# Optimization experiments

Measured on AMD Instinct MI355X. Metric: run time of the kernel, lower is better.

The kernel has to match this reference:

```python
import jax, jax.numpy as jnp
import numpy as np

B, IN, H, NC = 8192, 1024, 1024, 16
CS = H // NC  # chunk_size = 64


def cumsoftmax(x):
    # cumulative softmax along last dim
    return jnp.cumsum(jax.nn.softmax(x, axis=-1), axis=-1)


def setup_inputs() -> dict:
    key = jax.random.key(0)
    ks = jax.random.split(key, 9)
    s_ih = 1.0 / np.sqrt(IN)
    s_hh = 1.0 / np.sqrt(H)
    return {
        "x": jax.random.normal(ks[0], (B, IN), jnp.float32),
        "hx": jax.random.normal(ks[1], (B, H), jnp.float32),
        "cx": jax.random.normal(ks[2], (B, NC, CS), jnp.float32),
        "input_floor": jax.random.normal(ks[3], (B, NC), jnp.float32),
        "forget_floor": jax.random.normal(ks[4], (B, NC), jnp.float32),
        "W_ih": jax.random.uniform(ks[5], (4 * H, IN), jnp.float32, -s_ih, s_ih),
        "b_ih": jax.random.uniform(ks[6], (4 * H,), jnp.float32, -s_ih, s_ih),
        "W_hh": jax.random.uniform(ks[7], (4 * H, H), jnp.float32, -s_hh, s_hh),
        "b_hh": jax.random.uniform(ks[8], (4 * H,), jnp.float32, -s_hh, s_hh),
    }


def reference(x, hx, cx, input_floor, forget_floor, W_ih, b_ih, W_hh, b_hh):
    # dual GEMM (eval path: dropconnect=0.0 -> plain linear)
    gates = x @ W_ih.T + b_ih + hx @ W_hh.T + b_hh          # [B, 4H]
    g = gates.reshape(-1, NC * 4, CS)                        # [B, 4*NC, CS]
    outgate, cell, ingate, forgetgate = jnp.split(g, 4, axis=1)  # each [B, NC, CS]

    happy_in, sad_in = jnp.split(input_floor, 2, axis=1)     # [B, NC/2] each
    happy_fg, sad_fg = jnp.split(forget_floor, 2, axis=1)

    happy_cingate = cumsoftmax(happy_in)
    happy_cforgetgate = jnp.flip(cumsoftmax(jnp.flip(happy_fg, 1)), 1)
    sad_cingate = jnp.flip(cumsoftmax(jnp.flip(sad_in, 1)), 1)
    sad_cforgetgate = cumsoftmax(sad_fg)

    cingate = jnp.concatenate([happy_cingate, sad_cingate], axis=1)[:, :, None]      # [B, NC, 1]
    cforgetgate = jnp.concatenate([happy_cforgetgate, sad_cforgetgate], axis=1)[:, :, None]

    ingate = jax.nn.sigmoid(ingate)
    forgetgate = jax.nn.sigmoid(forgetgate)
    cell = jnp.tanh(cell)
    outgate = jax.nn.sigmoid(outgate)

    overlap = cforgetgate * cingate
    forgetgate = forgetgate * overlap + (cforgetgate - overlap)
    ingate = ingate * overlap + (cingate - overlap)

    cy = forgetgate * cx + ingate * cell                     # [B, NC, CS]
    hy = outgate * jnp.tanh(cy)
    return hy.reshape(-1, H), cy
```

## Files before the change

kernel.cpp:

```cpp
#include <hip/hip_runtime.h>
#include <hip/hip_bf16.h>


#define B_ROWS 8192
#define IN_DIM 1024
#define H_DIM  1024
#define NCHUNK 16
#define K_TOT  2048

#define BM   256
#define BN   256
#define BK   64
#define NKT  (K_TOT / BK)
#define THREADS 512

#define A_PACK_BYTES ((size_t)B_ROWS * K_TOT * 2)
#define W_PACK_BYTES ((size_t)16 * 256 * K_TOT * 2)

typedef __attribute__((ext_vector_type(4))) float  f32x4;
typedef __bf16 bf16x8 __attribute__((ext_vector_type(8)));

__device__ __forceinline__ float sigmoidf_(float x) {
    return 1.0f / (1.0f + __expf(-x));
}
__device__ __forceinline__ float tanhf_(float x) {
    float e = __expf(-2.0f * fabsf(x));
    float t = (1.0f - e) / (1.0f + e);
    return copysignf(t, x);
}

__device__ __forceinline__ void gload16(const __bf16* gsrc, __bf16* lds_dst) {
    __builtin_amdgcn_global_load_lds(
        (const __attribute__((address_space(1))) unsigned int*)gsrc,
        (__attribute__((address_space(3))) unsigned int*)lds_dst, 16, 0, 0);
}

__device__ __forceinline__ bf16x8 cvt8(f32x4 v0, f32x4 v1) {
    bf16x8 o;
    o[0] = (__bf16)v0.x; o[1] = (__bf16)v0.y; o[2] = (__bf16)v0.z; o[3] = (__bf16)v0.w;
    o[4] = (__bf16)v1.x; o[5] = (__bf16)v1.y; o[6] = (__bf16)v1.z; o[7] = (__bf16)v1.w;
    return o;
}

__global__ __launch_bounds__(256)
void pack_AW(const float* __restrict__ x, const float* __restrict__ hx,
             const float* __restrict__ W_ih, const float* __restrict__ W_hh,
             __bf16* __restrict__ Abf, __bf16* __restrict__ Wp)
{
    const int bid = blockIdx.x;
    const int c8  = threadIdx.x << 3;
    if (bid < B_ROWS) {
        const float* src = (c8 < IN_DIM)
            ? (x  + (size_t)bid * IN_DIM + c8)
            : (hx + (size_t)bid * IN_DIM + (c8 - IN_DIM));
        f32x4 v0 = *reinterpret_cast<const f32x4*>(src);
        f32x4 v1 = *reinterpret_cast<const f32x4*>(src + 4);
        *reinterpret_cast<bf16x8*>(Abf + (size_t)bid * K_TOT + c8) = cvt8(v0, v1);
    } else {
        const int r  = bid - B_ROWS;
        const int bh = r >> 8;
        const int n  = r & 255;
        const int g  = (n >> 4) & 3;
        const int j  = (n >> 6) * 16 + (n & 15);
        const int wr = g * H_DIM + bh * 64 + j;
        const float* src = (c8 < IN_DIM)
            ? (W_ih + (size_t)wr * IN_DIM + c8)
            : (W_hh + (size_t)wr * IN_DIM + (c8 - IN_DIM));
        f32x4 v0 = *reinterpret_cast<const f32x4*>(src);
        f32x4 v1 = *reinterpret_cast<const f32x4*>(src + 4);
        *reinterpret_cast<bf16x8*>(Wp + (size_t)r * K_TOT + c8) = cvt8(v0, v1);
    }
}

__device__ __forceinline__ void stage_half(const __bf16* __restrict__ gbase, int kb,
                                           __bf16* lbase, int row0, int tid) {
    #pragma unroll
    for (int i = 0; i < 2; ++i) {
        int e   = i * 4096 + tid * 8;
        int row = row0 + (e >> 6);
        int kd  = e & 63;
        gload16(gbase + (size_t)row * K_TOT + kb + (kd ^ ((row & 7) << 3)), lbase + e);
    }
}

#define SWZ(r, k) ((r) * 64 + ((k) ^ (((r) & 7) << 3)))

#define LDB(Bs) { \
    _Pragma("unroll") \
    for (int fn = 0; fn < 4; ++fn) { \
        int br = wcol + fn * 16 + lr; \
        bfr[fn][0] = *reinterpret_cast<const bf16x8*>(&(Bs)[SWZ(br, lh * 8)]); \
        bfr[fn][1] = *reinterpret_cast<const bf16x8*>(&(Bs)[SWZ(br, 32 + lh * 8)]); \
    } }

#define LDA(As, q) { \
    int ar = wrow + (q) * 32 + lr; \
    af[0][0] = *reinterpret_cast<const bf16x8*>(&(As)[SWZ(ar, lh * 8)]); \
    af[0][1] = *reinterpret_cast<const bf16x8*>(&(As)[SWZ(ar, 32 + lh * 8)]); \
    af[1][0] = *reinterpret_cast<const bf16x8*>(&(As)[SWZ(ar + 16, lh * 8)]); \
    af[1][1] = *reinterpret_cast<const bf16x8*>(&(As)[SWZ(ar + 16, 32 + lh * 8)]); \
    }

#define WBAR \
    asm volatile("s_waitcnt lgkmcnt(0)" ::: "memory"); \
    __builtin_amdgcn_sched_barrier(0); \
    __builtin_amdgcn_s_barrier(); \
    __builtin_amdgcn_sched_barrier(0);

#define WBARV \
    asm volatile("s_waitcnt lgkmcnt(0)" ::: "memory"); \
    asm volatile("s_waitcnt vmcnt(4)"   ::: "memory"); \
    __builtin_amdgcn_sched_barrier(0); \
    __builtin_amdgcn_s_barrier(); \
    __builtin_amdgcn_sched_barrier(0);

#define MF(q) { \
    __builtin_amdgcn_s_setprio(1); \
    _Pragma("unroll") \
    for (int ks = 0; ks < 2; ++ks) { \
        _Pragma("unroll") \
        for (int fn = 0; fn < 4; ++fn) { \
            acc[2*(q)][fn]   = __builtin_amdgcn_mfma_f32_16x16x32_bf16(af[0][ks], bfr[fn][ks], acc[2*(q)][fn],   0,0,0); \
            acc[2*(q)+1][fn] = __builtin_amdgcn_mfma_f32_16x16x32_bf16(af[1][ks], bfr[fn][ks], acc[2*(q)+1][fn], 0,0,0); \
        } \
    } \
    __builtin_amdgcn_s_setprio(0); \
    __builtin_amdgcn_sched_barrier(0); \
}

__global__ __launch_bounds__(THREADS, 2)
void onlstm_gemm8(const __bf16* __restrict__ Abf, const __bf16* __restrict__ Wp,
                  const float* __restrict__ cx,
                  const float* __restrict__ input_floor,
                  const float* __restrict__ forget_floor,
                  const float* __restrict__ b_ih, const float* __restrict__ b_hh,
                  float* __restrict__ out)
{
    __shared__ __align__(16) __bf16 lds[65536];
    __shared__ float ci_s[BM], cf_s[BM], bias_s[BN];

    const int tid = threadIdx.x;
    const int n0  = blockIdx.x;
    const int bm  = (n0 & 7) * 4 + ((n0 >> 3) & 3);
    const int bh  = n0 >> 5;
    const int h0  = bh * 64;
    const int nc  = bh;

    if (tid < BM) {
        {
            int g = (tid >> 4) & 3;
            int j = (tid >> 6) * 16 + (tid & 15);
            int wrr = g * H_DIM + h0 + j;
            bias_s[tid] = b_ih[wrr] + b_hh[wrr];
        }
        int b = bm * BM + tid;
        const int off = (nc < 8) ? 0 : 8;
        const int ic  = (nc < 8) ? nc : (nc - 8);
        const float* pin = input_floor  + (size_t)b * NCHUNK + off;
        const float* pfg = forget_floor + (size_t)b * NCHUNK + off;
        float vi[8], vf[8];
        float mi = -1e30f, mf = -1e30f;
        #pragma unroll
        for (int t = 0; t < 8; ++t) {
            vi[t] = pin[t]; vf[t] = pfg[t];
            mi = fmaxf(mi, vi[t]); mf = fmaxf(mf, vf[t]);
        }
        float si = 0.f, sf = 0.f;
        #pragma unroll
        for (int t = 0; t < 8; ++t) {
            vi[t] = __expf(vi[t] - mi); vf[t] = __expf(vf[t] - mf);
            si += vi[t]; sf += vf[t];
        }
        float pi = 0.f, pf = 0.f;
        #pragma unroll
        for (int t = 0; t < 8; ++t) { if (t <= ic) { pi += vi[t]; pf += vf[t]; } }
        float suf_i = si - pi + vi[ic];
        float suf_f = sf - pf + vf[ic];
        float civ, cfv;
        if (nc < 8) { civ = pi / si;    cfv = suf_f / sf; }
        else        { civ = suf_i / si; cfv = pf / sf;    }
        ci_s[tid] = civ; cf_s[tid] = cfv;
    }

    const __bf16* Arow = Abf + (size_t)(bm * BM) * K_TOT;
    const __bf16* Wblk = Wp  + (size_t)bh * 256 * K_TOT;
    __bf16* const A0p = lds;
    __bf16* const B0p = lds + 16384;
    __bf16* const A1p = lds + 32768;
    __bf16* const B1p = lds + 49152;

    stage_half(Arow, 0,  A0p,        0,   tid);
    stage_half(Arow, 0,  A0p + 8192, 128, tid);
    stage_half(Wblk, 0,  B0p,        0,   tid);
    stage_half(Wblk, 0,  B0p + 8192, 128, tid);
    stage_half(Wblk, BK, B1p,        0,   tid);
    stage_half(Wblk, BK, B1p + 8192, 128, tid);
    asm volatile("s_waitcnt lgkmcnt(0)" ::: "memory");
    asm volatile("s_waitcnt vmcnt(4)"   ::: "memory");
    __builtin_amdgcn_s_barrier();
    asm volatile("" ::: "memory");

    f32x4  acc[8][4];
    #pragma unroll
    for (int i = 0; i < 8; ++i)
        #pragma unroll
        for (int j = 0; j < 4; ++j) acc[i][j] = (f32x4){0.f, 0.f, 0.f, 0.f};
    bf16x8 af[2][2];
    bf16x8 bfr[4][2];

    const int l    = tid & 63;
    const int wid  = tid >> 6;
    const int wrw  = wid >> 2;
    const int wc   = wid & 3;
    const int lr   = l & 15;
    const int lh   = l >> 4;
    const int wrow = wrw * 128;
    const int wcol = wc * 64;

    #pragma unroll 1
    for (int it = 0; it < NKT / 2; ++it) {
        const int t = 2 * it;
        LDB(B0p); LDA(A0p, 0);
        stage_half(Arow, ((t + 1) & 31) * BK, A1p,        0,   tid);
        stage_half(Arow, ((t + 1) & 31) * BK, A1p + 8192, 128, tid);
        WBAR; MF(0);
        LDA(A0p, 1);
        stage_half(Wblk, ((t + 2) & 31) * BK, B0p,        0,   tid);
        WBAR; MF(1);
        LDA(A0p, 2);
        stage_half(Wblk, ((t + 2) & 31) * BK, B0p + 8192, 128, tid);
        WBAR; MF(2);
        LDA(A0p, 3);
        WBARV; MF(3);
        LDB(B1p); LDA(A1p, 0);
        stage_half(Arow, ((t + 2) & 31) * BK, A0p,        0,   tid);
        stage_half(Arow, ((t + 2) & 31) * BK, A0p + 8192, 128, tid);
        WBAR; MF(0);
        LDA(A1p, 1);
        stage_half(Wblk, ((t + 3) & 31) * BK, B1p,        0,   tid);
        WBAR; MF(1);
        LDA(A1p, 2);
        stage_half(Wblk, ((t + 3) & 31) * BK, B1p + 8192, 128, tid);
        WBAR; MF(2);
        LDA(A1p, 3);
        WBARV; MF(3);
    }
    asm volatile("s_waitcnt vmcnt(0)" ::: "memory");
    __builtin_amdgcn_s_barrier();

    const size_t CY_OFF = (size_t)B_ROWS * H_DIM;
    const int hcol = h0 + wc * 16 + lr;
    #pragma unroll
    for (int m = 0; m < 8; ++m) {
        #pragma unroll
        for (int r = 0; r < 4; ++r) {
            int rt = wrow + m * 16 + lh * 4 + r;
            int b  = bm * BM + rt;
            float civ = ci_s[rt], cfv = cf_s[rt];
            float ovl = cfv * civ;
            float og = acc[m][0][r] + bias_s[wcol + lr];
            float cg = acc[m][1][r] + bias_s[wcol + 16 + lr];
            float ig = acc[m][2][r] + bias_s[wcol + 32 + lr];
            float fg = acc[m][3][r] + bias_s[wcol + 48 + lr];
            float i_s = sigmoidf_(ig);
            float f_s = sigmoidf_(fg);
            float c_t = tanhf_(cg);
            float o_s = sigmoidf_(og);
            float fq = f_s * ovl + (cfv - ovl);
            float iq = i_s * ovl + (civ - ovl);
            float cxv = cx[(size_t)b * H_DIM + hcol];
            float cyv = fq * cxv + iq * c_t;
            float hyv = o_s * tanhf_(cyv);
            out[(size_t)b * H_DIM + hcol] = hyv;
            out[CY_OFF + (size_t)b * H_DIM + hcol] = cyv;
        }
    }
}

extern "C" void kernel_launch(void* const* d_in, const int* in_sizes, int n_in,
                              void* d_out, int out_size, void* d_ws, size_t ws_size,
                              hipStream_t stream) {
    const float* x            = (const float*)d_in[0];
    const float* hx           = (const float*)d_in[1];
    const float* cx           = (const float*)d_in[2];
    const float* input_floor  = (const float*)d_in[3];
    const float* forget_floor = (const float*)d_in[4];
    const float* W_ih         = (const float*)d_in[5];
    const float* b_ih         = (const float*)d_in[6];
    const float* W_hh         = (const float*)d_in[7];
    const float* b_hh         = (const float*)d_in[8];
    float* out = (float*)d_out;

    __bf16* Abf = (__bf16*)d_ws;
    __bf16* Wp  = (__bf16*)((char*)d_ws + A_PACK_BYTES);
    pack_AW<<<B_ROWS + 16 * 256, 256, 0, stream>>>(x, hx, W_ih, W_hh, Abf, Wp);
    onlstm_gemm8<<<512, THREADS, 0, stream>>>(
        Abf, Wp, cx, input_floor, forget_floor, b_ih, b_hh, out);
}
```

Baseline: 157.5 us.

## Switch GEMM to 32x32x16 MFMA with 4x2 warp layout and pipelined fragment loads

Replaces the 16x16x32 bf16 MFMA tiling with 32x32x16 instructions. Each of 8 waves now computes a 64x128 tile, and the weight packing and bias layout are permuted so each 32-column group holds one gate for 32 hidden units. B fragments are double-buffered in registers across k-substeps, and barriers use a partial lgkmcnt wait so LDS reads overlap the MFMAs. The goal is to cut LDS traffic per flop and raise matrix-core efficiency. The cost is more complex waitcnt accounting, which risks hazards, plus a different epilogue index mapping.

```diff
diff --git a/kernel.cpp b/kernel.cpp
--- a/kernel.cpp
+++ b/kernel.cpp
@@ -17,7 +17,8 @@
 #define A_PACK_BYTES ((size_t)B_ROWS * K_TOT * 2)
 #define W_PACK_BYTES ((size_t)16 * 256 * K_TOT * 2)
 
-typedef __attribute__((ext_vector_type(4))) float  f32x4;
+typedef __attribute__((ext_vector_type(4)))  float f32x4;
+typedef __attribute__((ext_vector_type(16))) float f32x16;
 typedef __bf16 bf16x8 __attribute__((ext_vector_type(8)));
 
 __device__ __forceinline__ float sigmoidf_(float x) {
@@ -60,8 +61,8 @@
         const int r  = bid - B_ROWS;
         const int bh = r >> 8;
         const int n  = r & 255;
-        const int g  = (n >> 4) & 3;
-        const int j  = (n >> 6) * 16 + (n & 15);
+        const int g  = (n >> 5) & 3;
+        const int j  = (n >> 7) * 32 + (n & 31);
         const int wr = g * H_DIM + bh * 64 + j;
         const float* src = (c8 < IN_DIM)
             ? (W_ih + (size_t)wr * IN_DIM + c8)
@@ -85,56 +86,53 @@
 
 #define SWZ(r, k) ((r) * 64 + ((k) ^ (((r) & 7) << 3)))
 
-#define LDB(Bs) { \
+#define LDA2(As, q) { \
+    int ar = wrow + c32; \
+    af[0] = *reinterpret_cast<const bf16x8*>(&(As)[SWZ(ar,      (q) * 16 + khi8)]); \
+    af[1] = *reinterpret_cast<const bf16x8*>(&(As)[SWZ(ar + 32, (q) * 16 + khi8)]); }
+
+#define LDB4(Bs, dst, ks) { \
     _Pragma("unroll") \
-    for (int fn = 0; fn < 4; ++fn) { \
-        int br = wcol + fn * 16 + lr; \
-        bfr[fn][0] = *reinterpret_cast<const bf16x8*>(&(Bs)[SWZ(br, lh * 8)]); \
-        bfr[fn][1] = *reinterpret_cast<const bf16x8*>(&(Bs)[SWZ(br, 32 + lh * 8)]); \
-    } }
-
-#define LDA(As, q) { \
-    int ar = wrow + (q) * 32 + lr; \
-    af[0][0] = *reinterpret_cast<const bf16x8*>(&(As)[SWZ(ar, lh * 8)]); \
-    af[0][1] = *reinterpret_cast<const bf16x8*>(&(As)[SWZ(ar, 32 + lh * 8)]); \
-    af[1][0] = *reinterpret_cast<const bf16x8*>(&(As)[SWZ(ar + 16, lh * 8)]); \
-    af[1][1] = *reinterpret_cast<const bf16x8*>(&(As)[SWZ(ar + 16, 32 + lh * 8)]); \
-    }
-
-#define WBAR \
-    asm volatile("s_waitcnt lgkmcnt(0)" ::: "memory"); \
+    for (int n = 0; n < 4; ++n) { \
+        int br = wcol + n * 32 + c32; \
+        dst[n] = *reinterpret_cast<const bf16x8*>(&(Bs)[SWZ(br, (ks) * 16 + khi8)]); } }
+
+#define WBARL \
+    asm volatile("s_waitcnt lgkmcnt(4)" ::: "memory"); \
     __builtin_amdgcn_sched_barrier(0); \
     __builtin_amdgcn_s_barrier(); \
     __builtin_amdgcn_sched_barrier(0);
 
-#define WBARV \
-    asm volatile("s_waitcnt lgkmcnt(0)" ::: "memory"); \
-    asm volatile("s_waitcnt vmcnt(4)"   ::: "memory"); \
+#define WBARLV4 \
+    asm volatile("s_waitcnt vmcnt(4) lgkmcnt(4)" ::: "memory"); \
     __builtin_amdgcn_sched_barrier(0); \
     __builtin_amdgcn_s_barrier(); \
     __builtin_amdgcn_sched_barrier(0);
 
-#define MF(q) { \
+#define WBARLV0 \
+    asm volatile("s_waitcnt vmcnt(0) lgkmcnt(4)" ::: "memory"); \
+    __builtin_amdgcn_sched_barrier(0); \
+    __builtin_amdgcn_s_barrier(); \
+    __builtin_amdgcn_sched_barrier(0);
+
+#define MF32(bsrc) { \
     __builtin_amdgcn_s_setprio(1); \
     _Pragma("unroll") \
-    for (int ks = 0; ks < 2; ++ks) { \
-        _Pragma("unroll") \
-        for (int fn = 0; fn < 4; ++fn) { \
-            acc[2*(q)][fn]   = __builtin_amdgcn_mfma_f32_16x16x32_bf16(af[0][ks], bfr[fn][ks], acc[2*(q)][fn],   0,0,0); \
-            acc[2*(q)+1][fn] = __builtin_amdgcn_mfma_f32_16x16x32_bf16(af[1][ks], bfr[fn][ks], acc[2*(q)+1][fn], 0,0,0); \
-        } \
+    for (int n = 0; n < 4; ++n) { \
+        acc[0][n] = __builtin_amdgcn_mfma_f32_32x32x16_bf16(af[0], bsrc[n], acc[0][n], 0, 0, 0); \
+        acc[1][n] = __builtin_amdgcn_mfma_f32_32x32x16_bf16(af[1], bsrc[n], acc[1][n], 0, 0, 0); \
     } \
     __builtin_amdgcn_s_setprio(0); \
     __builtin_amdgcn_sched_barrier(0); \
 }
 
 __global__ __launch_bounds__(THREADS, 2)
-void onlstm_gemm8(const __bf16* __restrict__ Abf, const __bf16* __restrict__ Wp,
-                  const float* __restrict__ cx,
-                  const float* __restrict__ input_floor,
-                  const float* __restrict__ forget_floor,
-                  const float* __restrict__ b_ih, const float* __restrict__ b_hh,
-                  float* __restrict__ out)
+void onlstm_gemm32(const __bf16* __restrict__ Abf, const __bf16* __restrict__ Wp,
+                   const float* __restrict__ cx,
+                   const float* __restrict__ input_floor,
+                   const float* __restrict__ forget_floor,
+                   const float* __restrict__ b_ih, const float* __restrict__ b_hh,
+                   float* __restrict__ out)
 {
     __shared__ __align__(16) __bf16 lds[65536];
     __shared__ float ci_s[BM], cf_s[BM], bias_s[BN];
@@ -148,8 +146,8 @@
 
     if (tid < BM) {
         {
-            int g = (tid >> 4) & 3;
-            int j = (tid >> 6) * 16 + (tid & 15);
+            int g = (tid >> 5) & 3;
+            int j = (tid >> 7) * 32 + (tid & 31);
             int wrr = g * H_DIM + h0 + j;
             bias_s[tid] = b_ih[wrr] + b_hh[wrr];
         }
@@ -189,79 +187,87 @@
     __bf16* const A1p = lds + 32768;
     __bf16* const B1p = lds + 49152;
 
-    stage_half(Arow, 0,  A0p,        0,   tid);
-    stage_half(Arow, 0,  A0p + 8192, 128, tid);
-    stage_half(Wblk, 0,  B0p,        0,   tid);
-    stage_half(Wblk, 0,  B0p + 8192, 128, tid);
-    stage_half(Wblk, BK, B1p,        0,   tid);
-    stage_half(Wblk, BK, B1p + 8192, 128, tid);
-    asm volatile("s_waitcnt lgkmcnt(0)" ::: "memory");
-    asm volatile("s_waitcnt vmcnt(4)"   ::: "memory");
+    const int l    = tid & 63;
+    const int wid  = tid >> 6;
+    const int wrw  = wid >> 1;
+    const int wc   = wid & 1;
+    const int c32  = l & 31;
+    const int khi8 = (l >> 5) * 8;
+    const int wrow = wrw * 64;
+    const int wcol = wc * 128;
+
+    stage_half(Wblk, 0, B0p,        0,   tid);
+    stage_half(Wblk, 0, B0p + 8192, 128, tid);
+    stage_half(Arow, 0, A0p,        0,   tid);
+    stage_half(Arow, 0, A0p + 8192, 128, tid);
+    asm volatile("s_waitcnt vmcnt(0) lgkmcnt(0)" ::: "memory");
     __builtin_amdgcn_s_barrier();
     asm volatile("" ::: "memory");
 
-    f32x4  acc[8][4];
+    f32x16 acc[2][4];
     #pragma unroll
-    for (int i = 0; i < 8; ++i)
-        #pragma unroll
-        for (int j = 0; j < 4; ++j) acc[i][j] = (f32x4){0.f, 0.f, 0.f, 0.f};
-    bf16x8 af[2][2];
-    bf16x8 bfr[4][2];
-
-    const int l    = tid & 63;
-    const int wid  = tid >> 6;
-    const int wrw  = wid >> 2;
-    const int wc   = wid & 3;
-    const int lr   = l & 15;
-    const int lh   = l >> 4;
-    const int wrow = wrw * 128;
-    const int wcol = wc * 64;
+    for (int i = 0; i < 2; ++i)
+        #pragma unroll
+        for (int j = 0; j < 4; ++j) acc[i][j] = (f32x16)(0.0f);
+    bf16x8 af[2];
+    bf16x8 bfr1[4], bfr2[4];
+
+    LDB4(B0p, bfr1, 0);
 
     #pragma unroll 1
     for (int it = 0; it < NKT / 2; ++it) {
         const int t = 2 * it;
-        LDB(B0p); LDA(A0p, 0);
+        LDA2(A0p, 0);
+        LDB4(B0p, bfr2, 1);
+        stage_half(Wblk, ((t + 1) & 31) * BK, B1p,        0,   tid);
+        stage_half(Wblk, ((t + 1) & 31) * BK, B1p + 8192, 128, tid);
         stage_half(Arow, ((t + 1) & 31) * BK, A1p,        0,   tid);
+        WBARL;   MF32(bfr1);
+        LDA2(A0p, 1);
+        LDB4(B0p, bfr1, 2);
         stage_half(Arow, ((t + 1) & 31) * BK, A1p + 8192, 128, tid);
-        WBAR; MF(0);
-        LDA(A0p, 1);
+        WBARL;   MF32(bfr2);
+        LDA2(A0p, 2);
+        LDB4(B0p, bfr2, 3);
+        WBARLV4; MF32(bfr1);
+        LDA2(A0p, 3);
+        LDB4(B1p, bfr1, 0);
+        WBARLV0; MF32(bfr2);
+        LDA2(A1p, 0);
+        LDB4(B1p, bfr2, 1);
         stage_half(Wblk, ((t + 2) & 31) * BK, B0p,        0,   tid);
-        WBAR; MF(1);
-        LDA(A0p, 2);
         stage_half(Wblk, ((t + 2) & 31) * BK, B0p + 8192, 128, tid);
-        WBAR; MF(2);
-        LDA(A0p, 3);
-        WBARV; MF(3);
-        LDB(B1p); LDA(A1p, 0);
         stage_half(Arow, ((t + 2) & 31) * BK, A0p,        0,   tid);
+        WBARL;   MF32(bfr1);
+        LDA2(A1p, 1);
+        LDB4(B1p, bfr1, 2);
         stage_half(Arow, ((t + 2) & 31) * BK, A0p + 8192, 128, tid);
-        WBAR; MF(0);
-        LDA(A1p, 1);
-        stage_half(Wblk, ((t + 3) & 31) * BK, B1p,        0,   tid);
-        WBAR; MF(1);
-        LDA(A1p, 2);
-        stage_half(Wblk, ((t + 3) & 31) * BK, B1p + 8192, 128, tid);
-        WBAR; MF(2);
-        LDA(A1p, 3);
-        WBARV; MF(3);
-    }
-    asm volatile("s_waitcnt vmcnt(0)" ::: "memory");
-    __builtin_amdgcn_s_barrier();
+        WBARL;   MF32(bfr2);
+        LDA2(A1p, 2);
+        LDB4(B1p, bfr2, 3);
+        WBARLV4; MF32(bfr1);
+        LDA2(A1p, 3);
+        LDB4(B0p, bfr1, 0);
+        WBARLV0; MF32(bfr2);
+    }
+    asm volatile("s_waitcnt vmcnt(0) lgkmcnt(0)" ::: "memory");
 
     const size_t CY_OFF = (size_t)B_ROWS * H_DIM;
-    const int hcol = h0 + wc * 16 + lr;
+    const int hcol = h0 + wc * 32 + c32;
+    const int rbase = (l >> 5) * 4;
     #pragma unroll
-    for (int m = 0; m < 8; ++m) {
-        #pragma unroll
-        for (int r = 0; r < 4; ++r) {
-            int rt = wrow + m * 16 + lh * 4 + r;
-            int b  = bm * BM + rt;
+    for (int mt = 0; mt < 2; ++mt) {
+        #pragma unroll
+        for (int reg = 0; reg < 16; ++reg) {
+            int r32 = (reg & 3) + 8 * (reg >> 2) + rbase;
+            int rt  = wrow + mt * 32 + r32;
+            int b   = bm * BM + rt;
             float civ = ci_s[rt], cfv = cf_s[rt];
             float ovl = cfv * civ;
-            float og = acc[m][0][r] + bias_s[wcol + lr];
-            float cg = acc[m][1][r] + bias_s[wcol + 16 + lr];
-            float ig = acc[m][2][r] + bias_s[wcol + 32 + lr];
-            float fg = acc[m][3][r] + bias_s[wcol + 48 + lr];
+            float og = acc[mt][0][reg] + bias_s[wcol + c32];
+            float cg = acc[mt][1][reg] + bias_s[wcol + 32 + c32];
+            float ig = acc[mt][2][reg] + bias_s[wcol + 64 + c32];
+            float fg = acc[mt][3][reg] + bias_s[wcol + 96 + c32];
             float i_s = sigmoidf_(ig);
             float f_s = sigmoidf_(fg);
             float c_t = tanhf_(cg);
@@ -294,6 +300,6 @@
     __bf16* Abf = (__bf16*)d_ws;
     __bf16* Wp  = (__bf16*)((char*)d_ws + A_PACK_BYTES);
     pack_AW<<<B_ROWS + 16 * 256, 256, 0, stream>>>(x, hx, W_ih, W_hh, Abf, Wp);
-    onlstm_gemm8<<<512, THREADS, 0, stream>>>(
+    onlstm_gemm32<<<512, THREADS, 0, stream>>>(
         Abf, Wp, cx, input_floor, forget_floor, b_ih, b_hh, out);
 }
```

Measured after the change: 172.1 us. 1.09x slower.
